# Kernel tuning notes

Measured on AMD Instinct MI355X. Metric: run time of the kernel, lower is better.

The kernel has to match this reference:

```python
import jax, jax.numpy as jnp
import numpy as np

B, SQ, SK, D, H = 8, 2048, 2048, 512, 8
QP, KP, VP = 512, 512, 4096  # VP must equal D*H for O_w to accept the concat


def setup_inputs() -> dict:
    key = jax.random.key(0)
    ks = jax.random.split(key, 9)
    q_in = jax.random.normal(ks[0], (B, SQ, D), dtype=jnp.float32)
    k_in = jax.random.normal(ks[1], (B, SK, D), dtype=jnp.float32)
    v_in = jax.random.normal(ks[2], (B, SK, D), dtype=jnp.float32)
    mask = jax.random.randint(ks[3], (B, SQ, SK), 0, 2, dtype=jnp.int32)
    W_q = jax.random.normal(ks[4], (D, QP), dtype=jnp.float32) * 0.02
    W_k = jax.random.normal(ks[5], (D, KP), dtype=jnp.float32) * 0.02
    W_v = jax.random.normal(ks[6], (D, VP), dtype=jnp.float32) * 0.02
    W_o = jax.random.normal(ks[7], (VP, D), dtype=jnp.float32) * 0.02
    b_o = jnp.zeros((D,), dtype=jnp.float32)
    return {"q_in": q_in, "k_in": k_in, "v_in": v_in,
            "W_q": W_q, "W_k": W_k, "W_v": W_v, "W_o": W_o, "b_o": b_o,
            "mask": mask}


def reference(q_in, k_in, v_in, W_q, W_k, W_v, W_o, b_o, mask):
    b, sq, d = q_in.shape
    sk = k_in.shape[1]
    # NOTE: original scales by sqrt(input_dim // num_heads), NOT actual head dim
    scale = jnp.asarray(np.sqrt(d // H), dtype=q_in.dtype)
    q = q_in @ W_q  # (B, Sq, QP)
    k = k_in @ W_k  # (B, Sk, KP)
    v = v_in @ W_v  # (B, Sk, VP)
    q_h = q.reshape(b, sq, H, -1).transpose(0, 2, 1, 3)  # (B,H,Sq,dq)
    k_h = k.reshape(b, sk, H, -1).transpose(0, 2, 1, 3)  # (B,H,Sk,dk)
    v_h = v.reshape(b, sk, H, -1).transpose(0, 2, 1, 3)  # (B,H,Sk,dv)
    attn = jnp.einsum('bhid,bhkd->bhik', q_h, k_h)  # (B,H,Sq,Sk)
    attn = jnp.where(mask[:, None, :, :] == 0, jnp.asarray(-1e9, attn.dtype), attn)
    attn = jax.nn.softmax(attn / scale, axis=-1)
    out = attn @ v_h  # (B,H,Sq,dv)
    # Faithful to original bug: transpose(0,1) swaps BATCH and HEAD, then reshape
    out = jnp.transpose(out, (1, 0, 2, 3)).reshape(b, sq, -1)  # (B,Sq,H*dv)
    return out @ W_o + b_o
```

## Files before the change

### kernel.cpp

```cpp
#include <hip/hip_runtime.h>
#include <math.h>

typedef __bf16 bf16x8 __attribute__((ext_vector_type(8)));
typedef float fx4 __attribute__((ext_vector_type(4)));
typedef unsigned short u16;
typedef unsigned short u16x8 __attribute__((ext_vector_type(8)));
typedef unsigned int u32;
typedef unsigned char u8;

__device__ __forceinline__ fx4 mfma16(bf16x8 a, bf16x8 b, fx4 c) {
  return __builtin_amdgcn_mfma_f32_16x16x32_bf16(a, b, c, 0, 0, 0);
}
__device__ __forceinline__ u16 f2bf(float f) {
  u32 u = __float_as_uint(f);
  u += 0x7fffu + ((u >> 16) & 1u);
  return (u16)(u >> 16);
}
__device__ __forceinline__ u16 bfc(float f) {
  __bf16 h = (__bf16)f;
  return __builtin_bit_cast(u16, h);
}
__device__ __forceinline__ float ex2(float x) { return __builtin_amdgcn_exp2f(x); }

#define BB 8
#define SS 2048
#define DD 512
#define HH 8
#define DQ 64
#define DV 512
#define VP 4096

#define OFF_QP  ((size_t)0)
#define OFF_KP  ((size_t)16777216)
#define OFF_WQT ((size_t)33554432)
#define OFF_WKT ((size_t)34078720)
#define OFF_WVT ((size_t)34603008)
#define OFF_WOT ((size_t)38797312)
#define OFF_MB  ((size_t)42991616)
#define OFF_VT  ((size_t)76546048)
#define OFF_XB  ((size_t)210763776)

__global__ __launch_bounds__(256) void transpose_w(const float* __restrict__ W,
                                                   u16* __restrict__ Wt,
                                                   int K, int N) {
  __shared__ float t[32][33];
  const int n0 = blockIdx.x * 32, k0 = blockIdx.y * 32;
  const int tx = threadIdx.x & 31, ty = threadIdx.x >> 5;
#pragma unroll
  for (int i = 0; i < 32; i += 8)
    t[ty + i][tx] = W[(size_t)(k0 + ty + i) * N + n0 + tx];
  __syncthreads();
#pragma unroll
  for (int i = 0; i < 32; i += 8)
    Wt[(size_t)(n0 + ty + i) * K + k0 + tx] = f2bf(t[tx][ty + i]);
}

__global__ __launch_bounds__(256) void mask_pack(const int* __restrict__ m,
                                                 u8* __restrict__ mb) {
  const size_t i = ((size_t)blockIdx.x * 256 + threadIdx.x) * 16;
  int4 a0 = *(const int4*)(m + i);
  int4 a1 = *(const int4*)(m + i + 4);
  int4 a2 = *(const int4*)(m + i + 8);
  int4 a3 = *(const int4*)(m + i + 12);
  uint4 o;
  o.x = (a0.x ? 1u : 0u) | ((a0.y ? 1u : 0u) << 8) | ((a0.z ? 1u : 0u) << 16) | ((a0.w ? 1u : 0u) << 24);
  o.y = (a1.x ? 1u : 0u) | ((a1.y ? 1u : 0u) << 8) | ((a1.z ? 1u : 0u) << 16) | ((a1.w ? 1u : 0u) << 24);
  o.z = (a2.x ? 1u : 0u) | ((a2.y ? 1u : 0u) << 8) | ((a2.z ? 1u : 0u) << 16) | ((a2.w ? 1u : 0u) << 24);
  o.w = (a3.x ? 1u : 0u) | ((a3.y ? 1u : 0u) << 8) | ((a3.z ? 1u : 0u) << 16) | ((a3.w ? 1u : 0u) << 24);
  *(uint4*)(mb + i) = o;
}

template <int AFP32, int EPI>
__global__ __launch_bounds__(256) void gemm_bt(const void* __restrict__ Ap,
                                               const u16* __restrict__ Bt,
                                               void* __restrict__ Cp,
                                               int M, int N, int K,
                                               const float* __restrict__ bias,
                                               float scale) {
  __shared__ union {
    struct { u16 As[128 * 32]; u16 Bs[128 * 32]; } s;
    u16 T[4][64 * 68];
  } sm;
  const int tid = threadIdx.x;
  const int lane = tid & 63, w = tid >> 6;
  const int lhi = lane >> 4, llo = lane & 15;
  const int wm = w >> 1, wn = w & 1;
  const int m0 = blockIdx.y * 128, n0 = blockIdx.x * 128;

  fx4 acc[4][4];
#pragma unroll
  for (int i = 0; i < 4; ++i)
#pragma unroll
    for (int j = 0; j < 4; ++j) acc[i][j] = (fx4){0.f, 0.f, 0.f, 0.f};

  for (int k0 = 0; k0 < K; k0 += 32) {
    if (AFP32) {
      const float* A = (const float*)Ap;
      const int row = tid >> 1, co = (tid & 1) * 16;
      const float* src = A + (size_t)(m0 + row) * K + k0 + co;
      float4 v0 = *(const float4*)(src + 0);
      float4 v1 = *(const float4*)(src + 4);
      float4 v2 = *(const float4*)(src + 8);
      float4 v3 = *(const float4*)(src + 12);
      u16x8 p0 = {f2bf(v0.x), f2bf(v0.y), f2bf(v0.z), f2bf(v0.w),
                  f2bf(v1.x), f2bf(v1.y), f2bf(v1.z), f2bf(v1.w)};
      u16x8 p1 = {f2bf(v2.x), f2bf(v2.y), f2bf(v2.z), f2bf(v2.w),
                  f2bf(v3.x), f2bf(v3.y), f2bf(v3.z), f2bf(v3.w)};
      *(u16x8*)&sm.s.As[row * 32 + co] = p0;
      *(u16x8*)&sm.s.As[row * 32 + co + 8] = p1;
    } else {
      const u16* A = (const u16*)Ap;
#pragma unroll
      for (int j = 0; j < 2; ++j) {
        int cc = j * 256 + tid;
        int row = cc >> 2, c8 = (cc & 3) * 8;
        *(uint4*)&sm.s.As[cc * 8] = *(const uint4*)&A[(size_t)(m0 + row) * K + k0 + c8];
      }
    }
#pragma unroll
    for (int j = 0; j < 2; ++j) {
      int cc = j * 256 + tid;
      int row = cc >> 2, c8 = (cc & 3) * 8;
      *(uint4*)&sm.s.Bs[cc * 8] = *(const uint4*)&Bt[(size_t)(n0 + row) * K + k0 + c8];
    }
    __syncthreads();
    bf16x8 af[4], bfv[4];
#pragma unroll
    for (int mi = 0; mi < 4; ++mi)
      af[mi] = *(const bf16x8*)&sm.s.As[(wm * 64 + mi * 16 + llo) * 32 + lhi * 8];
#pragma unroll
    for (int ni = 0; ni < 4; ++ni)
      bfv[ni] = *(const bf16x8*)&sm.s.Bs[(wn * 64 + ni * 16 + llo) * 32 + lhi * 8];
#pragma unroll
    for (int mi = 0; mi < 4; ++mi)
#pragma unroll
      for (int ni = 0; ni < 4; ++ni)
        acc[mi][ni] = mfma16(af[mi], bfv[ni], acc[mi][ni]);
    __syncthreads();
  }

  const int rbase = m0 + wm * 64, cbase = n0 + wn * 64;
  if (EPI == 0) {
    u16* C = (u16*)Cp;
#pragma unroll
    for (int mi = 0; mi < 4; ++mi) {
      int r0 = rbase + mi * 16 + lhi * 4;
#pragma unroll
      for (int ni = 0; ni < 4; ++ni) {
        int c = cbase + ni * 16 + llo;
#pragma unroll
        for (int r = 0; r < 4; ++r)
          C[(size_t)(r0 + r) * N + c] = f2bf(acc[mi][ni][r] * scale);
      }
    }
  } else if (EPI == 1) {
    u16* Tw = &sm.T[w][0];
#pragma unroll
    for (int mi = 0; mi < 4; ++mi)
#pragma unroll
      for (int ni = 0; ni < 4; ++ni) {
        ushort4 pk;
        pk.x = f2bf(acc[mi][ni][0]);
        pk.y = f2bf(acc[mi][ni][1]);
        pk.z = f2bf(acc[mi][ni][2]);
        pk.w = f2bf(acc[mi][ni][3]);
        *(ushort4*)&Tw[(ni * 16 + llo) * 68 + mi * 16 + lhi * 4] = pk;
      }
    u16* VtC = (u16*)Cp;
    const int bsel = rbase >> 11;
    const int sb = rbase & 2047;
    u16* dst = VtC + ((size_t)(bsel * VP + cbase + lane)) * SS + sb;
#pragma unroll
    for (int j = 0; j < 8; ++j) {
      u16x8 vv = *(u16x8*)&Tw[lane * 68 + j * 8];
      *(u16x8*)&dst[j * 8] = vv;
    }
  } else {
    float* C = (float*)Cp;
#pragma unroll
    for (int ni = 0; ni < 4; ++ni) {
      int c = cbase + ni * 16 + llo;
      float bv = bias[c];
#pragma unroll
      for (int mi = 0; mi < 4; ++mi) {
        int r0 = rbase + mi * 16 + lhi * 4;
#pragma unroll
        for (int r = 0; r < 4; ++r)
          C[(size_t)(r0 + r) * N + c] = acc[mi][ni][r] + bv;
      }
    }
  }
}

#define KB 128
__global__ __launch_bounds__(256, 3) void attn(const u16* __restrict__ Qp,
                                               const u16* __restrict__ Kp,
                                               const u16* __restrict__ Vt,
                                               const u8* __restrict__ mb,
                                               u16* __restrict__ Xb) {
  const int lin = blockIdx.x;
  const int xcd = lin & 7, idx = lin >> 3;
  const int chunk = idx >> 5, qt = idx & 31;
  const int b = chunk >> 1, dvh = chunk & 1, h = xcd;
  const int m0 = qt * 64;
  const int tid = threadIdx.x, w = tid >> 6, lane = tid & 63;
  const int lhi = lane >> 4, llo = lane & 15;
  const int xork = (llo & 7) << 4;

  __shared__ u16 Psm[2][64 * 128];
  __shared__ float sm_lw[4][64];
  __shared__ float sm_l[64];

  bf16x8 qf[4][2];
#pragma unroll
  for (int mt = 0; mt < 4; ++mt)
#pragma unroll
    for (int ks = 0; ks < 2; ++ks)
      qf[mt][ks] = *(const bf16x8*)&Qp[(size_t)(b * SS + m0 + mt * 16 + llo) * 512 +
                                       h * DQ + ks * 32 + lhi * 8];

  fx4 acc[4][4];
#pragma unroll
  for (int mt = 0; mt < 4; ++mt)
#pragma unroll
    for (int nt = 0; nt < 4; ++nt) acc[mt][nt] = (fx4){0.f, 0.f, 0.f, 0.f};
  float lp[4] = {0.f, 0.f, 0.f, 0.f};

  const size_t kbase = (size_t)(b * SS) * 512 + h * DQ + lhi * 8;
  const size_t vbase =
      (size_t)(b * VP + h * DV + dvh * 256 + w * 64 + llo) * SS + lhi * 8;
  const u8* mrow[4];
#pragma unroll
  for (int mt = 0; mt < 4; ++mt)
    mrow[mt] = mb + (size_t)(b * SS + m0 + mt * 16 + llo) * SS + w * 32 + lhi * 4;

  for (int n0 = 0; n0 < SS; n0 += KB) {
    const int buf = (n0 >> 7) & 1;
    char* Pb = (char*)&Psm[buf][0];

    bf16x8 kf[2][2];
#pragma unroll
    for (int st = 0; st < 2; ++st)
#pragma unroll
      for (int ks = 0; ks < 2; ++ks)
        kf[st][ks] = *(const bf16x8*)&Kp[kbase +
                                         (size_t)(n0 + w * 32 + st * 16 + llo) * 512 +
                                         ks * 32];
    u32 mv[4][2];
#pragma unroll
    for (int mt = 0; mt < 4; ++mt)
#pragma unroll
      for (int st = 0; st < 2; ++st)
        mv[mt][st] = *(const u32*)(mrow[mt] + n0 + st * 16);

#pragma unroll
    for (int mt = 0; mt < 4; ++mt) {
      const int qL = mt * 16 + llo;
      char* prow = Pb + qL * 256;
#pragma unroll
      for (int st = 0; st < 2; ++st) {
        fx4 s = (fx4){0.f, 0.f, 0.f, 0.f};
        s = mfma16(kf[st][0], qf[mt][0], s);
        s = mfma16(kf[st][1], qf[mt][1], s);
        const u32 m = mv[mt][st];
        float p0 = (m & 0x000000ffu) ? ex2(s[0]) : 0.f;
        float p1 = (m & 0x0000ff00u) ? ex2(s[1]) : 0.f;
        float p2 = (m & 0x00ff0000u) ? ex2(s[2]) : 0.f;
        float p3 = (m & 0xff000000u) ? ex2(s[3]) : 0.f;
        lp[mt] += (p0 + p1) + (p2 + p3);
        ushort4 pk = {bfc(p0), bfc(p1), bfc(p2), bfc(p3)};
        *(ushort4*)(prow + ((w * 64 + st * 32 + lhi * 8) ^ xork)) = pk;
      }
    }
    __syncthreads();

#pragma unroll
    for (int kk = 0; kk < 4; ++kk) {
      bf16x8 pf[4];
#pragma unroll
      for (int mt = 0; mt < 4; ++mt)
        pf[mt] = *(const bf16x8*)(Pb + (mt * 16 + llo) * 256 +
                                  ((kk * 64 + lhi * 16) ^ xork));
      __builtin_amdgcn_s_setprio(1);
#pragma unroll
      for (int nt = 0; nt < 4; ++nt) {
        bf16x8 vf = *(const bf16x8*)&Vt[vbase + (size_t)(nt * 16) * SS + n0 + kk * 32];
#pragma unroll
        for (int mt = 0; mt < 4; ++mt)
          acc[mt][nt] = mfma16(pf[mt], vf, acc[mt][nt]);
      }
      __builtin_amdgcn_s_setprio(0);
    }
  }

#pragma unroll
  for (int mt = 0; mt < 4; ++mt) {
    lp[mt] += __shfl_xor(lp[mt], 16);
    lp[mt] += __shfl_xor(lp[mt], 32);
  }
  if (lhi == 0) {
#pragma unroll
    for (int mt = 0; mt < 4; ++mt) sm_lw[w][mt * 16 + llo] = lp[mt];
  }
  __syncthreads();
  if (tid < 64)
    sm_l[tid] = (sm_lw[0][tid] + sm_lw[1][tid]) + (sm_lw[2][tid] + sm_lw[3][tid]);
  __syncthreads();

  float linv[4][4];
#pragma unroll
  for (int mt = 0; mt < 4; ++mt)
#pragma unroll
    for (int r = 0; r < 4; ++r) linv[mt][r] = 1.0f / sm_l[mt * 16 + lhi * 4 + r];

  u16* Xs = (u16*)&Psm[0][0];
  const int er = tid >> 4, ec = (tid & 15) * 16;
#pragma unroll
  for (int mt = 0; mt < 4; ++mt) {
#pragma unroll
    for (int nt = 0; nt < 4; ++nt)
#pragma unroll
      for (int r = 0; r < 4; ++r)
        Xs[(lhi * 4 + r) * 264 + w * 64 + nt * 16 + llo] =
            f2bf(acc[mt][nt][r] * linv[mt][r]);
    __syncthreads();
    {
      const u16* src = Xs + er * 264 + ec;
      u16* dst = Xb + (size_t)((h * 8 + b) * SS + m0 + mt * 16 + er) * 512 +
                 dvh * 256 + ec;
      uint4 a0 = *(const uint4*)(src + 0);
      uint4 a1 = *(const uint4*)(src + 8);
      *(uint4*)(dst + 0) = a0;
      *(uint4*)(dst + 8) = a1;
    }
    __syncthreads();
  }
}

extern "C" void kernel_launch(void* const* d_in, const int* in_sizes, int n_in,
                              void* d_out, int out_size, void* d_ws, size_t ws_size,
                              hipStream_t stream) {
  (void)in_sizes; (void)n_in; (void)out_size; (void)ws_size;
  const float* q_in = (const float*)d_in[0];
  const float* k_in = (const float*)d_in[1];
  const float* v_in = (const float*)d_in[2];
  const float* W_q  = (const float*)d_in[3];
  const float* W_k  = (const float*)d_in[4];
  const float* W_v  = (const float*)d_in[5];
  const float* W_o  = (const float*)d_in[6];
  const float* b_o  = (const float*)d_in[7];
  const int*   mask = (const int*)d_in[8];

  char* ws = (char*)d_ws;
  u16* Qp   = (u16*)(ws + OFF_QP);
  u16* Kp   = (u16*)(ws + OFF_KP);
  u16* Wqt  = (u16*)(ws + OFF_WQT);
  u16* Wkt  = (u16*)(ws + OFF_WKT);
  u16* Wvt  = (u16*)(ws + OFF_WVT);
  u16* Wot  = (u16*)(ws + OFF_WOT);
  u8*  Mb   = (u8*)(ws + OFF_MB);
  u16* Vt   = (u16*)(ws + OFF_VT);
  u16* Xb   = (u16*)(ws + OFF_XB);

  transpose_w<<<dim3(16, 16), 256, 0, stream>>>(W_q, Wqt, 512, 512);
  transpose_w<<<dim3(16, 16), 256, 0, stream>>>(W_k, Wkt, 512, 512);
  transpose_w<<<dim3(128, 16), 256, 0, stream>>>(W_v, Wvt, 512, 4096);
  transpose_w<<<dim3(16, 128), 256, 0, stream>>>(W_o, Wot, 4096, 512);
  mask_pack<<<dim3(8192), 256, 0, stream>>>(mask, Mb);

  gemm_bt<1, 0><<<dim3(4, 128), 256, 0, stream>>>(q_in, Wqt, Qp, 16384, 512, 512, nullptr, 0.18033688011112f);
  gemm_bt<1, 0><<<dim3(4, 128), 256, 0, stream>>>(k_in, Wkt, Kp, 16384, 512, 512, nullptr, 1.0f);
  gemm_bt<1, 1><<<dim3(32, 128), 256, 0, stream>>>(v_in, Wvt, Vt, 16384, 4096, 512, nullptr, 1.0f);

  attn<<<dim3(4096), 256, 0, stream>>>(Qp, Kp, Vt, Mb, Xb);

  gemm_bt<0, 2><<<dim3(4, 128), 256, 0, stream>>>(Xb, Wot, d_out, 16384, 512, 4096, b_o, 1.0f);
}
```

Measured before the change: 1.492 ms.

## Bit-pack mask and register-prefetch next K/V/mask tiles in attention

The mask is packed to one bit per element instead of one byte, cutting mask bytes read by the attention kernel. The attention loop now prefetches the next tile's K fragments, mask words and V fragments into registers while the current tile is processed, and the P staging buffer uses a padded per-wave layout instead of an XOR swizzle. The larger register footprint lowers the launch bound from 3 to 2 blocks per CU, trading occupancy for explicit latency hiding.

```diff
diff --git a/kernel.cpp b/kernel.cpp
--- a/kernel.cpp
+++ b/kernel.cpp
@@ -55,19 +55,20 @@
     Wt[(size_t)(n0 + ty + i) * K + k0 + tx] = f2bf(t[tx][ty + i]);
 }
 
-__global__ __launch_bounds__(256) void mask_pack(const int* __restrict__ m,
-                                                 u8* __restrict__ mb) {
-  const size_t i = ((size_t)blockIdx.x * 256 + threadIdx.x) * 16;
-  int4 a0 = *(const int4*)(m + i);
-  int4 a1 = *(const int4*)(m + i + 4);
-  int4 a2 = *(const int4*)(m + i + 8);
-  int4 a3 = *(const int4*)(m + i + 12);
-  uint4 o;
-  o.x = (a0.x ? 1u : 0u) | ((a0.y ? 1u : 0u) << 8) | ((a0.z ? 1u : 0u) << 16) | ((a0.w ? 1u : 0u) << 24);
-  o.y = (a1.x ? 1u : 0u) | ((a1.y ? 1u : 0u) << 8) | ((a1.z ? 1u : 0u) << 16) | ((a1.w ? 1u : 0u) << 24);
-  o.z = (a2.x ? 1u : 0u) | ((a2.y ? 1u : 0u) << 8) | ((a2.z ? 1u : 0u) << 16) | ((a2.w ? 1u : 0u) << 24);
-  o.w = (a3.x ? 1u : 0u) | ((a3.y ? 1u : 0u) << 8) | ((a3.z ? 1u : 0u) << 16) | ((a3.w ? 1u : 0u) << 24);
-  *(uint4*)(mb + i) = o;
+__global__ __launch_bounds__(256) void mask_packbits(const int* __restrict__ m,
+                                                     u32* __restrict__ mb) {
+  const size_t widx = (size_t)blockIdx.x * 256 + threadIdx.x;
+  const int* src = m + widx * 32;
+  u32 r = 0;
+#pragma unroll
+  for (int j = 0; j < 32; j += 4) {
+    int4 a = *(const int4*)(src + j);
+    r |= (a.x ? 1u : 0u) << j;
+    r |= (a.y ? 1u : 0u) << (j + 1);
+    r |= (a.z ? 1u : 0u) << (j + 2);
+    r |= (a.w ? 1u : 0u) << (j + 3);
+  }
+  mb[widx] = r;
 }
 
 template <int AFP32, int EPI>
@@ -193,10 +194,10 @@
 }
 
 #define KB 128
-__global__ __launch_bounds__(256, 3) void attn(const u16* __restrict__ Qp,
+__global__ __launch_bounds__(256, 2) void attn(const u16* __restrict__ Qp,
                                                const u16* __restrict__ Kp,
                                                const u16* __restrict__ Vt,
-                                               const u8* __restrict__ mb,
+                                               const u32* __restrict__ mb,
                                                u16* __restrict__ Xb) {
   const int lin = blockIdx.x;
   const int xcd = lin & 7, idx = lin >> 3;
@@ -205,9 +206,8 @@
   const int m0 = qt * 64;
   const int tid = threadIdx.x, w = tid >> 6, lane = tid & 63;
   const int lhi = lane >> 4, llo = lane & 15;
-  const int xork = (llo & 7) << 4;
-
-  __shared__ u16 Psm[2][64 * 128];
+
+  __shared__ u16 Psm[2][4][64][40];
   __shared__ float sm_lw[4][64];
   __shared__ float sm_l[64];
 
@@ -229,68 +229,89 @@
   const size_t kbase = (size_t)(b * SS) * 512 + h * DQ + lhi * 8;
   const size_t vbase =
       (size_t)(b * VP + h * DV + dvh * 256 + w * 64 + llo) * SS + lhi * 8;
-  const u8* mrow[4];
+  const u32* mrowp[4];
 #pragma unroll
   for (int mt = 0; mt < 4; ++mt)
-    mrow[mt] = mb + (size_t)(b * SS + m0 + mt * 16 + llo) * SS + w * 32 + lhi * 4;
+    mrowp[mt] = mb + (size_t)(b * SS + m0 + mt * 16 + llo) * 64 + w;
+  const u32 bm0 = 1u << (lhi * 4), bm1 = bm0 << 1, bm2 = bm0 << 2, bm3 = bm0 << 3;
+
+  bf16x8 kf[2][2];
+  u32 mvc[4];
+  bf16x8 vf[4][4];
+#pragma unroll
+  for (int st = 0; st < 2; ++st)
+#pragma unroll
+    for (int ks = 0; ks < 2; ++ks)
+      kf[st][ks] = *(const bf16x8*)&Kp[kbase +
+                                       (size_t)(w * 32 + st * 16 + llo) * 512 +
+                                       ks * 32];
+#pragma unroll
+  for (int mt = 0; mt < 4; ++mt) mvc[mt] = mrowp[mt][0];
+#pragma unroll
+  for (int kk = 0; kk < 4; ++kk)
+#pragma unroll
+    for (int nt = 0; nt < 4; ++nt)
+      vf[kk][nt] = *(const bf16x8*)&Vt[vbase + (size_t)(nt * 16) * SS + kk * 32];
 
   for (int n0 = 0; n0 < SS; n0 += KB) {
     const int buf = (n0 >> 7) & 1;
-    char* Pb = (char*)&Psm[buf][0];
-
-    bf16x8 kf[2][2];
-#pragma unroll
-    for (int st = 0; st < 2; ++st)
-#pragma unroll
-      for (int ks = 0; ks < 2; ++ks)
-        kf[st][ks] = *(const bf16x8*)&Kp[kbase +
-                                         (size_t)(n0 + w * 32 + st * 16 + llo) * 512 +
-                                         ks * 32];
-    u32 mv[4][2];
-#pragma unroll
-    for (int mt = 0; mt < 4; ++mt)
-#pragma unroll
-      for (int st = 0; st < 2; ++st)
-        mv[mt][st] = *(const u32*)(mrow[mt] + n0 + st * 16);
+    const int nn = (n0 + KB) & (SS - 1);
 
 #pragma unroll
     for (int mt = 0; mt < 4; ++mt) {
       const int qL = mt * 16 + llo;
-      char* prow = Pb + qL * 256;
+      u16* Pw = &Psm[buf][w][qL][0];
 #pragma unroll
       for (int st = 0; st < 2; ++st) {
         fx4 s = (fx4){0.f, 0.f, 0.f, 0.f};
         s = mfma16(kf[st][0], qf[mt][0], s);
         s = mfma16(kf[st][1], qf[mt][1], s);
-        const u32 m = mv[mt][st];
-        float p0 = (m & 0x000000ffu) ? ex2(s[0]) : 0.f;
-        float p1 = (m & 0x0000ff00u) ? ex2(s[1]) : 0.f;
-        float p2 = (m & 0x00ff0000u) ? ex2(s[2]) : 0.f;
-        float p3 = (m & 0xff000000u) ? ex2(s[3]) : 0.f;
+        const u32 mst = mvc[mt] >> (st * 16);
+        float p0 = (mst & bm0) ? ex2(s[0]) : 0.f;
+        float p1 = (mst & bm1) ? ex2(s[1]) : 0.f;
+        float p2 = (mst & bm2) ? ex2(s[2]) : 0.f;
+        float p3 = (mst & bm3) ? ex2(s[3]) : 0.f;
         lp[mt] += (p0 + p1) + (p2 + p3);
         ushort4 pk = {bfc(p0), bfc(p1), bfc(p2), bfc(p3)};
-        *(ushort4*)(prow + ((w * 64 + st * 32 + lhi * 8) ^ xork)) = pk;
-      }
-    }
-    __syncthreads();
-
+        *(ushort4*)&Pw[st * 16 + lhi * 4] = pk;
+      }
+    }
+
+    asm volatile("s_waitcnt lgkmcnt(0)" ::: "memory");
+    __builtin_amdgcn_s_barrier();
+    __builtin_amdgcn_sched_barrier(0);
+
+#pragma unroll
+    for (int st = 0; st < 2; ++st)
+#pragma unroll
+      for (int ks = 0; ks < 2; ++ks)
+        kf[st][ks] = *(const bf16x8*)&Kp[kbase +
+                                         (size_t)(nn + w * 32 + st * 16 + llo) * 512 +
+                                         ks * 32];
+#pragma unroll
+    for (int mt = 0; mt < 4; ++mt) mvc[mt] = mrowp[mt][nn >> 5];
+
+    const u16* Pb = &Psm[buf][0][0][0];
 #pragma unroll
     for (int kk = 0; kk < 4; ++kk) {
       bf16x8 pf[4];
 #pragma unroll
       for (int mt = 0; mt < 4; ++mt)
-        pf[mt] = *(const bf16x8*)(Pb + (mt * 16 + llo) * 256 +
-                                  ((kk * 64 + lhi * 16) ^ xork));
+        pf[mt] = *(const bf16x8*)&Pb[(size_t)(kk * 64 + mt * 16 + llo) * 40 + lhi * 8];
       __builtin_amdgcn_s_setprio(1);
 #pragma unroll
-      for (int nt = 0; nt < 4; ++nt) {
-        bf16x8 vf = *(const bf16x8*)&Vt[vbase + (size_t)(nt * 16) * SS + n0 + kk * 32];
+      for (int nt = 0; nt < 4; ++nt)
 #pragma unroll
         for (int mt = 0; mt < 4; ++mt)
-          acc[mt][nt] = mfma16(pf[mt], vf, acc[mt][nt]);
-      }
+          acc[mt][nt] = mfma16(pf[mt], vf[kk][nt], acc[mt][nt]);
       __builtin_amdgcn_s_setprio(0);
     }
+
+#pragma unroll
+    for (int kk = 0; kk < 4; ++kk)
+#pragma unroll
+      for (int nt = 0; nt < 4; ++nt)
+        vf[kk][nt] = *(const bf16x8*)&Vt[vbase + (size_t)(nt * 16) * SS + nn + kk * 32];
   }
 
 #pragma unroll
@@ -313,7 +334,7 @@
 #pragma unroll
     for (int r = 0; r < 4; ++r) linv[mt][r] = 1.0f / sm_l[mt * 16 + lhi * 4 + r];
 
-  u16* Xs = (u16*)&Psm[0][0];
+  u16* Xs = &Psm[0][0][0][0];
   const int er = tid >> 4, ec = (tid & 15) * 16;
 #pragma unroll
   for (int mt = 0; mt < 4; ++mt) {
@@ -358,7 +379,7 @@
   u16* Wkt  = (u16*)(ws + OFF_WKT);
   u16* Wvt  = (u16*)(ws + OFF_WVT);
   u16* Wot  = (u16*)(ws + OFF_WOT);
-  u8*  Mb   = (u8*)(ws + OFF_MB);
+  u32* Mb   = (u32*)(ws + OFF_MB);
   u16* Vt   = (u16*)(ws + OFF_VT);
   u16* Xb   = (u16*)(ws + OFF_XB);
 
@@ -366,7 +387,7 @@
   transpose_w<<<dim3(16, 16), 256, 0, stream>>>(W_k, Wkt, 512, 512);
   transpose_w<<<dim3(128, 16), 256, 0, stream>>>(W_v, Wvt, 512, 4096);
   transpose_w<<<dim3(16, 128), 256, 0, stream>>>(W_o, Wot, 4096, 512);
-  mask_pack<<<dim3(8192), 256, 0, stream>>>(mask, Mb);
+  mask_packbits<<<dim3(4096), 256, 0, stream>>>(mask, Mb);
 
   gemm_bt<1, 0><<<dim3(4, 128), 256, 0, stream>>>(q_in, Wqt, Qp, 16384, 512, 512, nullptr, 0.18033688011112f);
   gemm_bt<1, 0><<<dim3(4, 128), 256, 0, stream>>>(k_in, Wkt, Kp, 16384, 512, 512, nullptr, 1.0f);
```

After: 1.320 ms. 1.13x faster.
